# Kernel tuning notes

Hardware: AMD Instinct MI355X
Metric: run time of the kernel (lower is better)

## Reference

```python
import jax, jax.numpy as jnp
import numpy as np

HIDDEN = 1024
NUM_HEADS = 16
HEAD_DIM = HIDDEN // NUM_HEADS  # 64
MLP_HIDDEN = 4096
RMS_EPS = 1e-6


def setup_inputs() -> dict:
    key = jax.random.key(0)
    ks = jax.random.split(key, 4)
    B, L = 2, 2048
    x = jax.random.normal(ks[0], (B, L, HIDDEN), dtype=jnp.float32)
    pe = jax.random.normal(ks[1], (1, 1, L, HEAD_DIM // 2, 2, 2), dtype=jnp.float32)
    W1 = jax.random.normal(ks[2], (HIDDEN, 3 * HIDDEN + MLP_HIDDEN), dtype=jnp.float32) * (HIDDEN ** -0.5)
    b1 = jnp.zeros((3 * HIDDEN + MLP_HIDDEN,), dtype=jnp.float32)
    W2 = jax.random.normal(ks[3], (HIDDEN + MLP_HIDDEN, HIDDEN), dtype=jnp.float32) * ((HIDDEN + MLP_HIDDEN) ** -0.5)
    b2 = jnp.zeros((HIDDEN,), dtype=jnp.float32)
    q_scale = jnp.ones((HEAD_DIM,), dtype=jnp.float32)
    k_scale = jnp.ones((HEAD_DIM,), dtype=jnp.float32)
    return {"x": x, "pe": pe, "W1": W1, "b1": b1, "W2": W2, "b2": b2,
            "q_scale": q_scale, "k_scale": k_scale}


def _rms_norm(t, scale):
    # RMSNorm over last dim (head_dim) with learnable scale (flux QKNorm)
    rrms = jax.lax.rsqrt(jnp.mean(jnp.square(t), axis=-1, keepdims=True) + RMS_EPS)
    return t * rrms * scale


def _apply_rope(xq, xk, pe):
    # pe: [1,1,L,D/2,2,2]; x*: [B,H,L,D]
    def rope(t):
        t_ = t.reshape(*t.shape[:-1], -1, 1, 2)  # [B,H,L,D/2,1,2]
        out = pe[..., 0] * t_[..., 0] + pe[..., 1] * t_[..., 1]  # [B,H,L,D/2,2]
        return out.reshape(*t.shape)
    return rope(xq), rope(xk)


def reference(x, pe, W1, b1, W2, b2, q_scale, k_scale):
    B, L, _ = x.shape
    h = x @ W1 + b1  # [B,L,3H+Mh]
    qkv, mlp = h[..., : 3 * HIDDEN], h[..., 3 * HIDDEN:]
    # 'B L (K H D) -> K B H L D'
    qkv = qkv.reshape(B, L, 3, NUM_HEADS, HEAD_DIM).transpose(2, 0, 3, 1, 4)
    q, k, v = qkv[0], qkv[1], qkv[2]
    q = _rms_norm(q, q_scale)
    k = _rms_norm(k, k_scale)
    q, k = _apply_rope(q, k, pe)
    scale = HEAD_DIM ** -0.5
    scores = jnp.einsum('bhqd,bhkd->bhqk', q, k) * scale
    attn = jnp.einsum('bhqk,bhkd->bhqd', jax.nn.softmax(scores, axis=-1), v)
    attn = attn.transpose(0, 2, 1, 3).reshape(B, L, HIDDEN)  # 'B H L D -> B L (H D)'
    out = jnp.concatenate((attn, jax.nn.gelu(mlp)), axis=2) @ W2 + b2
    return out
```

## Files before the change

### kernel.cpp

```cpp
#include <hip/hip_runtime.h>

typedef __bf16 bf16;
typedef __bf16 bf16x8 __attribute__((ext_vector_type(8)));
typedef float f32x4 __attribute__((ext_vector_type(4)));
typedef float f32x16 __attribute__((ext_vector_type(16)));

#define GLDS16(gp, lp) __builtin_amdgcn_global_load_lds( \
    (__attribute__((address_space(1))) void*)(gp), \
    (__attribute__((address_space(3))) void*)(lp), 16, 0, 0)

__device__ inline float ex2(float x) { return exp2f(x); }

__device__ inline float gelu_fast(float x) {
    float t = ex2(-2.3022081702f * (x + 0.044715f * x * x * x));
    return x * __builtin_amdgcn_rcpf(1.0f + t);
}

__global__ __launch_bounds__(256) void prep_kernel(const float* __restrict__ x,
                                                   bf16* __restrict__ xb,
                                                   const float* __restrict__ W1,
                                                   bf16* __restrict__ w1t,
                                                   const float* __restrict__ W2,
                                                   bf16* __restrict__ w2t) {
    int bid = blockIdx.x;
    if (bid < 4096) {
        long i = ((long)bid * 256 + threadIdx.x) * 4;
        float4 v = *(const float4*)&x[i];
        xb[i + 0] = (bf16)v.x;
        xb[i + 1] = (bf16)v.y;
        xb[i + 2] = (bf16)v.z;
        xb[i + 3] = (bf16)v.w;
        return;
    }
    const float* W;
    bf16* WT;
    int K, N, n0, k0;
    if (bid < 11264) {
        int t = bid - 4096;
        W = W1; WT = w1t; K = 1024; N = 7168;
        n0 = (t % 224) * 32; k0 = (t / 224) * 32;
    } else {
        int t = bid - 11264;
        W = W2; WT = w2t; K = 5120; N = 1024;
        n0 = (t % 32) * 32; k0 = (t / 32) * 32;
    }
    __shared__ float tile[32][33];
    int tx = threadIdx.x & 31;
    int ty = threadIdx.x >> 5;
#pragma unroll
    for (int i = 0; i < 4; ++i)
        tile[ty + i * 8][tx] = W[(long)(k0 + ty + i * 8) * N + n0 + tx];
    __syncthreads();
#pragma unroll
    for (int i = 0; i < 4; ++i)
        WT[(long)(n0 + ty + i * 8) * K + k0 + tx] = (bf16)tile[tx][ty + i * 8];
}

__global__ __launch_bounds__(256) void gemm1_fused(const bf16* __restrict__ A,
                                                   const bf16* __restrict__ BT,
                                                   const float* __restrict__ bias,
                                                   const float* __restrict__ pe,
                                                   const float* __restrict__ qsc,
                                                   const float* __restrict__ ksc,
                                                   bf16* __restrict__ qb_,
                                                   bf16* __restrict__ kb_,
                                                   bf16* __restrict__ vsrc,
                                                   bf16* __restrict__ cat,
                                                   int K) {
    __shared__ __align__(16) char Asm[128 * 128];
    __shared__ __align__(16) char Bsm[128 * 128];
    int tid = threadIdx.x;
    int w = tid >> 6, l = tid & 63;
    int wr = w >> 1, wc = w & 1;
    int bm = blockIdx.x * 128;
    int bn = blockIdx.y * 128;

    f32x4 acc[4][4] = {};

    int fr = l & 15;
    int g16 = (l >> 4) * 16;
    int xsw = (fr & 7) << 4;

    int srow = tid >> 3;
    int sg8 = ((tid & 7) ^ (srow & 7)) * 8;
    int dstoff = tid * 16;

    int nk = K >> 6;
    for (int kt = 0; kt < nk; ++kt) {
        int k0 = kt * 64;
#pragma unroll
        for (int gg = 0; gg < 4; ++gg) {
            const bf16* ga = A + (long)(bm + gg * 32 + srow) * K + k0 + sg8;
            GLDS16(ga, Asm + gg * 4096 + dstoff);
            const bf16* gb = BT + (long)(bn + gg * 32 + srow) * K + k0 + sg8;
            GLDS16(gb, Bsm + gg * 4096 + dstoff);
        }
        asm volatile("s_waitcnt vmcnt(0)" ::: "memory");
        __syncthreads();

#pragma unroll
        for (int kk = 0; kk < 2; ++kk) {
            int koff = (kk * 64 + g16) ^ xsw;
            bf16x8 af[4], bfr[4];
#pragma unroll
            for (int m = 0; m < 4; ++m)
                af[m] = *(const bf16x8*)(Asm + (wr * 64 + m * 16 + fr) * 128 + koff);
#pragma unroll
            for (int n = 0; n < 4; ++n)
                bfr[n] = *(const bf16x8*)(Bsm + (wc * 64 + n * 16 + fr) * 128 + koff);
#pragma unroll
            for (int m = 0; m < 4; ++m)
#pragma unroll
                for (int n = 0; n < 4; ++n)
                    acc[m][n] = __builtin_amdgcn_mfma_f32_16x16x32_bf16(af[m], bfr[n], acc[m][n], 0, 0, 0);
        }
        __syncthreads();
    }

    int orow0 = bm + wr * 64;
    int ocol0 = bn + wc * 64;

    if (bn < 2048) {
        bool isq = (bn < 1024);
        const float* sc = isq ? qsc : ksc;
        bf16* dst = isq ? qb_ : kb_;
#pragma unroll
        for (int m = 0; m < 4; ++m) {
#pragma unroll
            for (int r = 0; r < 4; ++r) {
                int row = orow0 + m * 16 + (l >> 4) * 4 + r;
                int lpos = row & 2047;
                int bb = row >> 11;
                float v[4];
                float ss = 0.0f;
#pragma unroll
                for (int n = 0; n < 4; ++n) {
                    int col = ocol0 + n * 16 + fr;
                    v[n] = acc[m][n][r] + bias[col];
                    ss += v[n] * v[n];
                }
#pragma unroll
                for (int off = 1; off < 16; off <<= 1)
                    ss += __shfl_xor(ss, off, 16);
                float rr = rsqrtf(ss * (1.0f / 64.0f) + 1e-6f);
#pragma unroll
                for (int n = 0; n < 4; ++n) {
                    int col = ocol0 + n * 16 + fr;
                    int d = col & 63;
                    int hh = (col & 1023) >> 6;
                    float qn = v[n] * rr * sc[d];
                    float pv = __shfl_xor(qn, 1, 16);
                    float qe = (d & 1) ? pv : qn;
                    float qo = (d & 1) ? qn : pv;
                    float pe0 = pe[lpos * 128 + (d >> 1) * 4 + (d & 1) * 2 + 0];
                    float pe1 = pe[lpos * 128 + (d >> 1) * 4 + (d & 1) * 2 + 1];
                    float ov = pe0 * qe + pe1 * qo;
                    if (isq) ov *= 0.18033688011112042f;
                    dst[((long)(bb * 16 + hh) * 2048 + lpos) * 64 + d] = (bf16)ov;
                }
            }
        }
    } else if (bn < 3072) {
#pragma unroll
        for (int m = 0; m < 4; ++m) {
            int row = orow0 + m * 16 + (l >> 4) * 4;
#pragma unroll
            for (int n = 0; n < 4; ++n) {
                int col = ocol0 + n * 16 + fr;
                float bv = bias[col];
#pragma unroll
                for (int r = 0; r < 4; ++r)
                    vsrc[(long)(row + r) * 1024 + col - 2048] = (bf16)(acc[m][n][r] + bv);
            }
        }
    } else {
#pragma unroll
        for (int m = 0; m < 4; ++m) {
            int row = orow0 + m * 16 + (l >> 4) * 4;
#pragma unroll
            for (int n = 0; n < 4; ++n) {
                int col = ocol0 + n * 16 + fr;
                float bv = bias[col];
#pragma unroll
                for (int r = 0; r < 4; ++r) {
                    float v = acc[m][n][r] + bv;
                    cat[(long)(row + r) * 5120 + 1024 + col - 3072] = (bf16)gelu_fast(v);
                }
            }
        }
    }
}

#define STA(tile, ch) if ((tile) < NT) { \
    const bf16* s_ = gA + (tile) * 64 + (ch) * 32; \
    char* d_ = lds + ((tile) & 1) * 65536 + (ch) * 16384 + tid * 16; \
    GLDS16(s_, d_); GLDS16(s_ + (long)128 * K, d_ + 8192); }

#define STB(tile, ch) if ((tile) < NT) { \
    const bf16* s_ = gB + (tile) * 64 + (ch) * 32; \
    char* d_ = lds + ((tile) & 1) * 65536 + 32768 + (ch) * 16384 + tid * 16; \
    GLDS16(s_, d_); GLDS16(s_ + (long)128 * K, d_ + 8192); }

#define PH(tb, mh, kh, RB, STAGE_STMT, WAITN) do { \
    { const char* Ab_ = lds + (tb) * 65536 + (kh) * 16384; \
      const char* Bb_ = lds + (tb) * 65536 + 32768 + (kh) * 16384; \
      if (RB) { \
        _Pragma("unroll") for (int n_ = 0; n_ < 4; ++n_) \
          bfrag[n_] = *(const bf16x8*)(Bb_ + (wc * 64 + n_ * 16 + fr) * 64 + aslot); } \
      _Pragma("unroll") for (int i_ = 0; i_ < 4; ++i_) \
          afrag[i_] = *(const bf16x8*)(Ab_ + (wr * 128 + (mh) * 64 + i_ * 16 + fr) * 64 + aslot); \
    } \
    STAGE_STMT; \
    asm volatile("s_waitcnt vmcnt(" #WAITN ")" ::: "memory"); \
    asm volatile("s_barrier" ::: "memory"); \
    __builtin_amdgcn_s_setprio(1); \
    _Pragma("unroll") for (int n_ = 0; n_ < 4; ++n_) \
      _Pragma("unroll") for (int i_ = 0; i_ < 4; ++i_) \
        acc[(mh) * 4 + i_][n_] = __builtin_amdgcn_mfma_f32_16x16x32_bf16(afrag[i_], bfrag[n_], acc[(mh) * 4 + i_][n_], 0, 0, 0); \
    __builtin_amdgcn_s_setprio(0); \
    asm volatile("s_barrier" ::: "memory"); \
} while (0)

__global__ __launch_bounds__(512, 2) void gemm8p_sk(const bf16* __restrict__ A_,
                                                    const bf16* __restrict__ BT_,
                                                    bf16* __restrict__ part,
                                                    int M, int N, int K, int kch) {
    __shared__ __align__(16) char lds[131072];

    int bx = blockIdx.x, by = blockIdx.y;
    int k0base = blockIdx.z * kch;
    int bm = bx * 256, bn = by * 256;
    int NT = kch >> 6;

    int tid = threadIdx.x;
    int w = tid >> 6, l = tid & 63;
    int wr = w >> 2, wc = w & 3;
    int fr = l & 15;
    int aslot = (((l >> 4) ^ ((fr >> 1) & 3)) << 4);

    int srow0 = tid >> 2;
    int sgoff = (((tid & 3) ^ ((srow0 >> 1) & 3)) << 3);
    const bf16* gA = A_ + (long)(bm + srow0) * K + k0base + sgoff;
    const bf16* gB = BT_ + (long)(bn + srow0) * K + k0base + sgoff;

    f32x4 acc[8][4] = {};
    bf16x8 bfrag[4];
    bf16x8 afrag[4];

    STA(0, 0); STA(0, 1); STB(0, 0); STB(0, 1);
    STB(1, 0); STA(1, 0); STB(1, 1);
    asm volatile("s_waitcnt vmcnt(0)" ::: "memory");
    asm volatile("s_barrier" ::: "memory");

    int NI = NT >> 1;
    for (int i = 0; i < NI; ++i) {
        int t1 = 2 * i + 1, t2 = 2 * i + 2, t3 = 2 * i + 3;
        if (i == NI - 1) {
            PH(0, 0, 0, true, STA(t1, 1), 0);
        } else {
            PH(0, 0, 0, true, STA(t1, 1), 10);
        }
        PH(0, 1, 0, false, STB(t2, 0), 10);
        PH(0, 0, 1, true,  STA(t2, 0), 10);
        PH(0, 1, 1, false, STB(t2, 1), 10);
        PH(1, 0, 0, true,  STA(t2, 1), 10);
        PH(1, 1, 0, false, STB(t3, 0), 10);
        PH(1, 0, 1, true,  STA(t3, 0), 10);
        PH(1, 1, 1, false, STB(t3, 1), 10);
    }

    bf16* cz = part + (long)blockIdx.z * M * N;
    int r4 = (l >> 4) * 4;
#pragma unroll
    for (int mi = 0; mi < 8; ++mi) {
        int row = bm + wr * 128 + mi * 16 + r4;
#pragma unroll
        for (int n = 0; n < 4; ++n) {
            int col = bn + wc * 64 + n * 16 + fr;
#pragma unroll
            for (int r = 0; r < 4; ++r)
                cz[(long)(row + r) * N + col] = (bf16)acc[mi][n][r];
        }
    }
}

__global__ __launch_bounds__(256) void reduce4_kernel(const bf16* __restrict__ part,
                                                      const float* __restrict__ b2,
                                                      float* __restrict__ out) {
    const long stride = 4096L * 1024;
    long e0 = ((long)blockIdx.x * 256 + threadIdx.x) * 8;
    float s[8];
    int boff = (int)(e0 & 1023);
#pragma unroll
    for (int j = 0; j < 8; ++j) s[j] = b2[boff + j];
#pragma unroll
    for (int z = 0; z < 4; ++z) {
        bf16x8 v = *(const bf16x8*)&part[z * stride + e0];
#pragma unroll
        for (int j = 0; j < 8; ++j) s[j] += (float)v[j];
    }
    *(float4*)&out[e0] = *(float4*)&s[0];
    *(float4*)&out[e0 + 4] = *(float4*)&s[4];
}

__global__ __launch_bounds__(256) void vtrans_kernel(const bf16* __restrict__ vsrc,
                                                     bf16* __restrict__ vT) {
    __shared__ unsigned short tile[64 * 65];
    int bh = blockIdx.x;
    int b = bh >> 4, hh = bh & 15;
    int l0 = blockIdx.y * 64;
    int tid = threadIdx.x;

    int r = tid >> 3, c = tid & 7;
#pragma unroll
    for (int p = 0; p < 2; ++p) {
        int row = r + p * 32;
        const bf16* src = vsrc + (long)(b * 2048 + l0 + row) * 1024 + hh * 64 + c * 8;
        bf16x8 v = *(const bf16x8*)src;
        union { bf16x8 v; unsigned short s[8]; } u; u.v = v;
#pragma unroll
        for (int e = 0; e < 8; ++e) tile[row * 65 + c * 8 + e] = u.s[e];
    }
    __syncthreads();
#pragma unroll
    for (int p = 0; p < 2; ++p) {
        int idx = tid + p * 256;
        int d = idx >> 3, kg = idx & 7;
        union { bf16x8 v; unsigned short s[8]; } u;
#pragma unroll
        for (int e = 0; e < 8; ++e) u.s[e] = tile[(kg * 8 + e) * 65 + d];
        *(bf16x8*)&vT[((long)bh * 64 + d) * 2048 + l0 + kg * 8] = u.v;
    }
}

__global__ __launch_bounds__(256) void attn_kernel(const bf16* __restrict__ qg,
                                                   const bf16* __restrict__ kg_,
                                                   const bf16* __restrict__ vT,
                                                   bf16* __restrict__ cat) {
    __shared__ __align__(16) char lds[65536];

    int bidx = blockIdx.x;
    int bh = bidx & 31;
    int qblk = bidx >> 5;
    int b = bh >> 4, hh = bh & 15;
    int tid = threadIdx.x;
    int wv = tid >> 6, l = tid & 63;
    int h = l >> 5, ln = l & 31;
    int sw = (ln & 7) << 4;

    char* Pw = lds + 49152 + wv * 4096;

    const bf16* qbase = qg + ((long)bh * 2048 + qblk * 128 + wv * 32 + ln) * 64 + h * 8;
    bf16x8 qf[4];
#pragma unroll
    for (int ds = 0; ds < 4; ++ds) qf[ds] = *(const bf16x8*)(qbase + ds * 16);

    f32x16 Oa0 = {}, Oa1 = {};
    float lsum = 0.0f;

    int kr = tid >> 3, kg = tid & 7;
    int swb = (kg * 16) ^ ((kr & 7) << 4);
    const bf16* gK = kg_ + ((long)bh * 2048 + kr) * 64 + kg * 8;
    const bf16* gV = vT + ((long)bh * 64 + kr) * 2048 + kg * 8;

    bf16x8 rk0 = *(const bf16x8*)gK;
    bf16x8 rk1 = *(const bf16x8*)(gK + 32 * 64);
    bf16x8 rv0 = *(const bf16x8*)gV;
    bf16x8 rv1 = *(const bf16x8*)(gV + 32 * 2048);
    *(bf16x8*)(lds + kr * 128 + swb) = rk0;
    *(bf16x8*)(lds + (kr + 32) * 128 + swb) = rk1;
    *(bf16x8*)(lds + 24576 + kr * 128 + swb) = rv0;
    *(bf16x8*)(lds + 24576 + (kr + 32) * 128 + swb) = rv1;
    __syncthreads();

    int bufR = 0;
    for (int t = 0; t < 32; ++t) {
        if (t < 31) {
            rk0 = *(const bf16x8*)(gK + (long)(t + 1) * 4096);
            rk1 = *(const bf16x8*)(gK + (long)(t + 1) * 4096 + 32 * 64);
            rv0 = *(const bf16x8*)(gV + (t + 1) * 64);
            rv1 = *(const bf16x8*)(gV + (t + 1) * 64 + 32 * 2048);
        }
        const char* Kc = lds + bufR * 8192;
        const char* Vc = lds + 24576 + bufR * 8192;

        f32x16 S0 = {}, S1 = {};
        __builtin_amdgcn_s_setprio(1);
#pragma unroll
        for (int ds = 0; ds < 4; ++ds) {
            bf16x8 kf0 = *(const bf16x8*)(Kc + ln * 128 + ((ds * 32 + h * 16) ^ sw));
            bf16x8 kf1 = *(const bf16x8*)(Kc + (32 + ln) * 128 + ((ds * 32 + h * 16) ^ sw));
            S0 = __builtin_amdgcn_mfma_f32_32x32x16_bf16(kf0, qf[ds], S0, 0, 0, 0);
            S1 = __builtin_amdgcn_mfma_f32_32x32x16_bf16(kf1, qf[ds], S1, 0, 0, 0);
        }
        __builtin_amdgcn_s_setprio(0);

#pragma unroll
        for (int kvt = 0; kvt < 2; ++kvt) {
            float p[16];
#pragma unroll
            for (int r = 0; r < 16; ++r) {
                float v = ex2((kvt ? S1[r] : S0[r]) - 12.0f);
                p[r] = v;
                lsum += v;
            }
#pragma unroll
            for (int j = 0; j < 4; ++j) {
                union { bf16 bb[4]; unsigned u[2]; } pr;
                pr.bb[0] = (bf16)p[4 * j];
                pr.bb[1] = (bf16)p[4 * j + 1];
                pr.bb[2] = (bf16)p[4 * j + 2];
                pr.bb[3] = (bf16)p[4 * j + 3];
                int base = 16 * j + 8 * h + 64 * kvt;
                *(unsigned long long*)(Pw + ln * 128 + (base ^ sw)) =
                    ((unsigned long long)pr.u[1] << 32) | pr.u[0];
            }
        }

        asm volatile("s_waitcnt lgkmcnt(0)" ::: "memory");

        bf16x8 pa[4];
#pragma unroll
        for (int s = 0; s < 4; ++s)
            pa[s] = *(const bf16x8*)(Pw + ln * 128 + ((s * 32 + h * 16) ^ sw));

        __builtin_amdgcn_s_setprio(1);
#pragma unroll
        for (int s = 0; s < 4; ++s) {
            bf16x8 vf0 = *(const bf16x8*)(Vc + ln * 128 + ((s * 32 + h * 16) ^ sw));
            bf16x8 vf1 = *(const bf16x8*)(Vc + (32 + ln) * 128 + ((s * 32 + h * 16) ^ sw));
            Oa0 = __builtin_amdgcn_mfma_f32_32x32x16_bf16(pa[s], vf0, Oa0, 0, 0, 0);
            Oa1 = __builtin_amdgcn_mfma_f32_32x32x16_bf16(pa[s], vf1, Oa1, 0, 0, 0);
        }
        __builtin_amdgcn_s_setprio(0);

        if (t < 31) {
            int bufW = (bufR == 2) ? 0 : bufR + 1;
            *(bf16x8*)(lds + bufW * 8192 + kr * 128 + swb) = rk0;
            *(bf16x8*)(lds + bufW * 8192 + (kr + 32) * 128 + swb) = rk1;
            *(bf16x8*)(lds + 24576 + bufW * 8192 + kr * 128 + swb) = rv0;
            *(bf16x8*)(lds + 24576 + bufW * 8192 + (kr + 32) * 128 + swb) = rv1;
        }
        __syncthreads();
        bufR = (bufR == 2) ? 0 : bufR + 1;
    }

    lsum += __shfl_xor(lsum, 32, 64);

#pragma unroll
    for (int r = 0; r < 16; ++r) {
        int rowq = (r & 3) + 8 * (r >> 2) + 4 * h;
        float ls = __shfl(lsum, rowq, 64);
        float inv = 1.0f / ls;
        long trow = (long)b * 2048 + qblk * 128 + wv * 32 + rowq;
        cat[trow * 5120 + hh * 64 + ln] = (bf16)(Oa0[r] * inv);
        cat[trow * 5120 + hh * 64 + 32 + ln] = (bf16)(Oa1[r] * inv);
    }
}


extern "C" void kernel_launch(void* const* d_in, const int* in_sizes, int n_in,
                              void* d_out, int out_size, void* d_ws, size_t ws_size,
                              hipStream_t stream) {
    const float* x  = (const float*)d_in[0];
    const float* pe = (const float*)d_in[1];
    const float* W1 = (const float*)d_in[2];
    const float* b1 = (const float*)d_in[3];
    const float* W2 = (const float*)d_in[4];
    const float* b2 = (const float*)d_in[5];
    const float* qs = (const float*)d_in[6];
    const float* ks = (const float*)d_in[7];
    float* out = (float*)d_out;

    char* ws = (char*)d_ws;
    bf16* xb   = (bf16*)(ws);
    bf16* w1t  = (bf16*)(ws + 8388608);
    bf16* w2t  = (bf16*)(ws + 23068672);
    bf16* vsrc = (bf16*)(ws + 33554432);
    bf16* qb   = (bf16*)(ws + 92274688);
    bf16* kb   = (bf16*)(ws + 100663296);
    bf16* vT   = (bf16*)(ws + 109051904);
    bf16* cat  = (bf16*)(ws + 117440512);
    bf16* part = (bf16*)(ws + 33554432);

    prep_kernel<<<16384, 256, 0, stream>>>(x, xb, W1, w1t, W2, w2t);

    gemm1_fused<<<dim3(32, 56), 256, 0, stream>>>(xb, w1t, b1, pe, qs, ks,
                                                  qb, kb, vsrc, cat, 1024);

    vtrans_kernel<<<dim3(32, 32), 256, 0, stream>>>(vsrc, vT);

    attn_kernel<<<512, 256, 0, stream>>>(qb, kb, vT, cat);

    gemm8p_sk<<<dim3(16, 4, 4), 512, 0, stream>>>(cat, w2t, part, 4096, 1024, 5120, 1280);
    reduce4_kernel<<<2048, 256, 0, stream>>>(part, b2, out);
}
```

Before: 242.5 us.

## Build attention P fragments in registers via permlane swaps; swizzle GEMM1 block order

```diff
diff --git a/kernel.cpp b/kernel.cpp
--- a/kernel.cpp
+++ b/kernel.cpp
@@ -14,6 +14,20 @@
 __device__ inline float gelu_fast(float x) {
     float t = ex2(-2.3022081702f * (x + 0.044715f * x * x * x));
     return x * __builtin_amdgcn_rcpf(1.0f + t);
+}
+
+__device__ inline void plswap(int h, unsigned& a, unsigned& b) {
+#if __has_builtin(__builtin_amdgcn_permlane32_swap)
+    typedef unsigned u32x2_ __attribute__((ext_vector_type(2)));
+    u32x2_ r = __builtin_amdgcn_permlane32_swap(a, b, false, false);
+    a = r[0]; b = r[1];
+#else
+    unsigned sa = (unsigned)__shfl_xor((int)a, 32, 64);
+    unsigned sb = (unsigned)__shfl_xor((int)b, 32, 64);
+    unsigned na = h ? sb : a;
+    unsigned nb = h ? b : sa;
+    a = na; b = nb;
+#endif
 }
 
 __global__ __launch_bounds__(256) void prep_kernel(const float* __restrict__ x,
@@ -72,8 +86,10 @@
     int tid = threadIdx.x;
     int w = tid >> 6, l = tid & 63;
     int wr = w >> 1, wc = w & 1;
-    int bm = blockIdx.x * 128;
-    int bn = blockIdx.y * 128;
+    int bid = blockIdx.x;
+    int swz = (bid & 7) * 224 + (bid >> 3);
+    int bm = (swz & 31) * 128;
+    int bn = (swz >> 5) * 128;
 
     f32x4 acc[4][4] = {};
 
@@ -337,7 +353,7 @@
                                                    const bf16* __restrict__ kg_,
                                                    const bf16* __restrict__ vT,
                                                    bf16* __restrict__ cat) {
-    __shared__ __align__(16) char lds[65536];
+    __shared__ __align__(16) char lds[49152];
 
     int bidx = blockIdx.x;
     int bh = bidx & 31;
@@ -347,8 +363,6 @@
     int wv = tid >> 6, l = tid & 63;
     int h = l >> 5, ln = l & 31;
     int sw = (ln & 7) << 4;
-
-    char* Pw = lds + 49152 + wv * 4096;
 
     const bf16* qbase = qg + ((long)bh * 2048 + qblk * 128 + wv * 32 + ln) * 64 + h * 8;
     bf16x8 qf[4];
@@ -395,34 +409,38 @@
         }
         __builtin_amdgcn_s_setprio(0);
 
-#pragma unroll
-        for (int kvt = 0; kvt < 2; ++kvt) {
+        bf16x8 pa[4];
+#pragma unroll
+        for (int H = 0; H < 2; ++H) {
             float p[16];
 #pragma unroll
             for (int r = 0; r < 16; ++r) {
-                float v = ex2((kvt ? S1[r] : S0[r]) - 12.0f);
+                float v = ex2((H ? S1[r] : S0[r]) - 12.0f);
                 p[r] = v;
                 lsum += v;
             }
-#pragma unroll
-            for (int j = 0; j < 4; ++j) {
-                union { bf16 bb[4]; unsigned u[2]; } pr;
-                pr.bb[0] = (bf16)p[4 * j];
-                pr.bb[1] = (bf16)p[4 * j + 1];
-                pr.bb[2] = (bf16)p[4 * j + 2];
-                pr.bb[3] = (bf16)p[4 * j + 3];
-                int base = 16 * j + 8 * h + 64 * kvt;
-                *(unsigned long long*)(Pw + ln * 128 + (base ^ sw)) =
-                    ((unsigned long long)pr.u[1] << 32) | pr.u[0];
+            unsigned w0[4], w1[4];
+#pragma unroll
+            for (int tt = 0; tt < 4; ++tt) {
+                union { bf16 bb[2]; unsigned u; } pk0, pk1;
+                pk0.bb[0] = (bf16)p[4 * tt + 0];
+                pk0.bb[1] = (bf16)p[4 * tt + 1];
+                pk1.bb[0] = (bf16)p[4 * tt + 2];
+                pk1.bb[1] = (bf16)p[4 * tt + 3];
+                w0[tt] = pk0.u;
+                w1[tt] = pk1.u;
             }
-        }
-
-        asm volatile("s_waitcnt lgkmcnt(0)" ::: "memory");
-
-        bf16x8 pa[4];
-#pragma unroll
-        for (int s = 0; s < 4; ++s)
-            pa[s] = *(const bf16x8*)(Pw + ln * 128 + ((s * 32 + h * 16) ^ sw));
+#pragma unroll
+            for (int sp = 0; sp < 2; ++sp) {
+                unsigned A0 = w0[2 * sp], B0 = w0[2 * sp + 1];
+                unsigned A1 = w1[2 * sp], B1 = w1[2 * sp + 1];
+                plswap(h, A0, B0);
+                plswap(h, A1, B1);
+                union { unsigned u[4]; bf16x8 v; } pk;
+                pk.u[0] = A0; pk.u[1] = A1; pk.u[2] = B0; pk.u[3] = B1;
+                pa[H * 2 + sp] = pk.v;
+            }
+        }
 
         __builtin_amdgcn_s_setprio(1);
 #pragma unroll
@@ -485,8 +503,8 @@
 
     prep_kernel<<<16384, 256, 0, stream>>>(x, xb, W1, w1t, W2, w2t);
 
-    gemm1_fused<<<dim3(32, 56), 256, 0, stream>>>(xb, w1t, b1, pe, qs, ks,
-                                                  qb, kb, vsrc, cat, 1024);
+    gemm1_fused<<<dim3(1792), 256, 0, stream>>>(xb, w1t, b1, pe, qs, ks,
+                                                qb, kb, vsrc, cat, 1024);
 
     vtrans_kernel<<<dim3(32, 32), 256, 0, stream>>>(vsrc, vT);
 
```

Result: slower. 253.7 us (+4.6%).
